# Performance work log

Measured on AMD Instinct MI355X. Metric: run time of the kernel, lower is better.

Reference implementation:

```python
import jax, jax.numpy as jnp
import numpy as np

IN_DIM, HID, E, N = 1024, 2048, 8, 16384

def setup_inputs() -> dict:
    key = jax.random.key(0)
    ks = jax.random.split(key, 12)
    s_in = 1.0 / np.sqrt(IN_DIM)
    s_h = 1.0 / np.sqrt(HID)
    return {
        "x": jax.random.normal(ks[0], (N, IN_DIM), dtype=jnp.float32),
        "enc_W": jax.random.uniform(ks[1], (IN_DIM, HID), jnp.float32, -s_in, s_in),
        "enc_b": jax.random.uniform(ks[2], (HID,), jnp.float32, -s_in, s_in),
        "gate_W": jax.random.uniform(ks[3], (HID, E), jnp.float32, -s_h, s_h),
        "expert_W": jax.random.uniform(ks[4], (E, HID, HID), jnp.float32, -s_h, s_h),
        "expert_b": jax.random.uniform(ks[5], (E, HID), jnp.float32, -s_h, s_h),
        "res_W": jax.random.uniform(ks[6], (HID, HID), jnp.float32, -s_h, s_h),
        "res_b": jax.random.uniform(ks[7], (HID,), jnp.float32, -s_h, s_h),
        "coef_W": jax.random.uniform(ks[8], (HID, 2), jnp.float32, -s_h, s_h),
        "coef_b": jax.random.uniform(ks[9], (2,), jnp.float32, -s_h, s_h),
        "dec_W": jax.random.uniform(ks[10], (HID, IN_DIM), jnp.float32, -s_h, s_h),
        "dec_b": jax.random.uniform(ks[11], (IN_DIM,), jnp.float32, -s_h, s_h),
    }

def reference(x, enc_W, enc_b, gate_W, expert_W, expert_b, res_W, res_b, coef_W, coef_b, dec_W, dec_b):
    # Encode: Linear + ReLU -> h [N, HID]
    h = jax.nn.relu(x @ enc_W + enc_b)
    # Top-1 gating (softmax probs, argmax expert, combine weight = chosen prob)
    probs = jax.nn.softmax(h @ gate_W, axis=-1)          # [N, E]
    idx = jnp.argmax(probs, axis=-1)                     # [N]
    gate = jnp.max(probs, axis=-1, keepdims=True)        # [N, 1]
    # Dense dispatch: run every expert, select via one-hot combine
    y_all = jnp.einsum('nd,edh->neh', h, expert_W) + expert_b  # [N, E, HID]
    onehot = jax.nn.one_hot(idx, y_all.shape[1], dtype=h.dtype)
    moe_out = jnp.einsum('neh,ne->nh', y_all, onehot) * gate   # [N, HID]
    # Residual expert + learned 2-way blending coefficient
    res = h @ res_W + res_b
    coef = jax.nn.softmax(h @ coef_W + coef_b, axis=-1)        # [N, 2]
    out = moe_out * coef[:, 0:1] + res * coef[:, 1:2]
    # Decode
    return out @ dec_W + dec_b
```

## Files before the change

### kernel.cpp

```cpp
#include <hip/hip_runtime.h>


#define N_TOK 16384
#define IN_DIM 1024
#define HID 2048
#define NEXP 8
#define TAU 8.0e-3f

typedef __bf16 bf16_t;
typedef __bf16 bf16x8 __attribute__((ext_vector_type(8)));
typedef __bf16 bf16x4v __attribute__((ext_vector_type(4)));
typedef float f32x4 __attribute__((ext_vector_type(4)));
typedef unsigned short ushort_t;

#define CLAMP1E4(v) fmaxf(fminf((v), 1.0e4f), -1.0e4f)

#define ASYNC16(gp, lp)                                                        \
  __builtin_amdgcn_global_load_lds(                                            \
      (const __attribute__((address_space(1))) void*)(gp),                     \
      (__attribute__((address_space(3))) void*)(lp), 16, 0, 0)

static __device__ inline ushort_t b2u(bf16_t v) {
  union { bf16_t b; ushort_t u; } x; x.b = v; return x.u;
}
// ... 70 lines not shown
    case 5: gWb[i] = (bf16_t)v; break;
    default: cWb[i] = (bf16_t)v; break;
  }
}

__global__ __launch_bounds__(256) void transpose_cvt(
    const void* __restrict__ src0, ushort_t* __restrict__ dst, int R, int C,
    size_t elem_off, const int* __restrict__ flagp, size_t src_zstride,
    size_t dst_zstride) {
  __shared__ ushort_t t[32][33];
  const int f = *flagp;
  const size_t eoff = elem_off + (size_t)blockIdx.z * src_zstride;
  dst += (size_t)blockIdx.z * dst_zstride;
  const int c0 = blockIdx.x * 32, r0 = blockIdx.y * 32;
  const int tx = threadIdx.x, ty = threadIdx.y;
  if (f) {
    const float* s = (const float*)src0 + eoff;
#pragma unroll
    for (int i = 0; i < 4; ++i)
      t[ty + i * 8][tx] =
          b2u((bf16_t)s[(size_t)(r0 + ty + i * 8) * C + c0 + tx]);
  } else {
    const ushort_t* s = (const ushort_t*)src0 + eoff;
#pragma unroll
    for (int i = 0; i < 4; ++i)
      t[ty + i * 8][tx] = s[(size_t)(r0 + ty + i * 8) * C + c0 + tx];
  }
  __syncthreads();
#pragma unroll
  for (int i = 0; i < 4; ++i)
    dst[(size_t)(c0 + ty + i * 8) * R + r0 + tx] = t[tx][ty + i * 8];
}

__global__ __launch_bounds__(256) void enc_gemm(
    const bf16_t* __restrict__ A, const bf16_t* __restrict__ Bt,
    const float* __restrict__ bias, bf16_t* __restrict__ H) {
  __shared__ bf16_t As[128 * 32];
  __shared__ bf16_t Bs[128 * 32];

  const int tid = threadIdx.x, lane = tid & 63, w = tid >> 6;
  const int wr = w >> 1, wc = w & 1, quad = lane >> 4, l16 = lane & 15;
  const int m0 = blockIdx.x * 128, n0 = blockIdx.y * 128;
  const char* Ab = (const char*)A;
  const char* Bb = (const char*)Bt;
  const size_t lda = (size_t)IN_DIM * 2;

  const f32x4 fz = {0.f, 0.f, 0.f, 0.f};
  f32x4 acc[4][4];
#pragma unroll
  for (int i = 0; i < 4; ++i)
#pragma unroll
    for (int j = 0; j < 4; ++j) acc[i][j] = fz;

  size_t aoff[2], boff[2];
  int cb[2];
#pragma unroll
  for (int c = 0; c < 2; ++c) {
    cb[c] = (w * 2 + c) * 1024;
    const int o = cb[c] + lane * 16;
    const int row = o >> 6, kb = o & 63;
    aoff[c] = (size_t)(m0 + row) * lda + kb;
    boff[c] = (size_t)(n0 + row) * lda + kb;
  }

  for (int kt = 0; kt < IN_DIM / 32; ++kt) {
    __syncthreads();
#pragma unroll
    for (int c = 0; c < 2; ++c) {
      ASYNC16(Ab + aoff[c] + (size_t)kt * 64, (char*)As + cb[c]);
      ASYNC16(Bb + boff[c] + (size_t)kt * 64, (char*)Bs + cb[c]);
    }
    __syncthreads();

    bf16x8 af[4], bfr[4];
#pragma unroll
    for (int i = 0; i < 4; ++i)
      af[i] = *(const bf16x8*)&As[(wr * 64 + i * 16 + l16) * 32 + quad * 8];
#pragma unroll
    for (int j = 0; j < 4; ++j)
      bfr[j] = *(const bf16x8*)&Bs[(wc * 64 + j * 16 + l16) * 32 + quad * 8];
#pragma unroll
    for (int i = 0; i < 4; ++i)
#pragma unroll
      for (int j = 0; j < 4; ++j)
        acc[i][j] = __builtin_amdgcn_mfma_f32_16x16x32_bf16(af[i], bfr[j],
                                                            acc[i][j], 0, 0, 0);
  }

  float bj[4];
  int colj[4];
#pragma unroll
  for (int j = 0; j < 4; ++j) {
    colj[j] = n0 + wc * 64 + j * 16 + l16;
    bj[j] = bias[colj[j]];
  }

#pragma unroll
  for (int i = 0; i < 4; ++i) {
#pragma unroll
    for (int r = 0; r < 4; ++r) {
      const int row = m0 + wr * 64 + i * 16 + quad * 4 + r;
#pragma unroll
      for (int j = 0; j < 4; ++j) {
        const float v = fminf(fmaxf(acc[i][j][r] + bj[j], 0.f), 1.0e4f);
        H[(size_t)row * HID + colj[j]] = (bf16_t)v;
      }
    }
  }
}

__global__ __launch_bounds__(256) void gate_from_h(
    const bf16_t* __restrict__ H, const bf16_t* __restrict__ gW,
    const bf16_t* __restrict__ cW, const float* __restrict__ coefBf,
    float* __restrict__ s0g, float* __restrict__ s1g, float* __restrict__ c0g,
    int* __restrict__ eidx, int* __restrict__ ambig, int* __restrict__ acnt,
    int* __restrict__ cnt) {
  const int tid = threadIdx.x, lane = tid & 63, w = tid >> 6;
  const int r0 = blockIdx.x * 16 + w * 4;

// ... 59 lines not shown
#pragma unroll
      for (int e = 0; e < 8; ++e) s += expf(lv[e] - mx);
      const float gate = 1.f / s;
      const float c0 = acc[g][8] + coefBf[0], c1 = acc[g][9] + coefBf[1];
      const float cm = fmaxf(c0, c1);
      const float e0 = expf(c0 - cm), e1 = expf(c1 - cm);
      const float inv = 1.f / (e0 + e1);
      const float p0 = e0 * inv;
      c0g[r] = p0;
      s1g[r] = e1 * inv;
      s0g[r] = gate * p0;
      eidx[r] = idx;
      atomicAdd(&cnt[idx], 1);
      if (mx - s2 < TAU) {
        const int p = atomicAdd(acnt, 1);
        ambig[p] = r;
      }
    }
  }
}

__global__ __launch_bounds__(256) void rescue_rows(
    const void* __restrict__ xraw, const void* __restrict__ encWraw,
    const float* __restrict__ encBf, const void* __restrict__ gateWraw,
    const int* __restrict__ flagp, const int* __restrict__ ambig,
    const int* __restrict__ acnt, const float* __restrict__ c0g,
    float* __restrict__ s0g, int* __restrict__ eidx, int* __restrict__ cnt) {
  const int i = blockIdx.x;
  if (i >= *acnt) return;
  const int r = ambig[i];
  const int f = *flagp;
  const int tid = threadIdx.x;

  double hacc[8] = {0, 0, 0, 0, 0, 0, 0, 0};
  if (f) {
    const float* x = (const float*)xraw + (size_t)r * IN_DIM;
    const float* W = (const float*)encWraw;
    for (int k = 0; k < IN_DIM; ++k) {
      const double xv = (double)x[k];
      const float* Wr = W + (size_t)k * HID;
#pragma unroll
      for (int jj = 0; jj < 8; ++jj)
        hacc[jj] += xv * (double)Wr[tid + jj * 256];
    }
  } else {
    const bf16_t* x = (const bf16_t*)xraw + (size_t)r * IN_DIM;
    const bf16_t* W = (const bf16_t*)encWraw;
    for (int k = 0; k < IN_DIM; ++k) {
      const double xv = (double)(float)x[k];
      const bf16_t* Wr = W + (size_t)k * HID;
#pragma unroll
      for (int jj = 0; jj < 8; ++jj)
        hacc[jj] += xv * (double)(float)Wr[tid + jj * 256];
    }
  }

  double lg[8] = {0, 0, 0, 0, 0, 0, 0, 0};
#pragma unroll
  for (int jj = 0; jj < 8; ++jj) {
    const int j = tid + jj * 256;
    double h = hacc[jj] + (double)encBf[j];
    if (h > 0.0) {
      if (f) {
        const float* g = (const float*)gateWraw + (size_t)j * 8;
#pragma unroll
        for (int e = 0; e < 8; ++e) lg[e] += h * (double)g[e];
      } else {
        const bf16_t* g = (const bf16_t*)gateWraw + (size_t)j * 8;
#pragma unroll
        for (int e = 0; e < 8; ++e) lg[e] += h * (double)(float)g[e];
      }
    }
  }
#pragma unroll
  for (int m = 1; m < 64; m <<= 1)
#pragma unroll
    for (int e = 0; e < 8; ++e) lg[e] += __shfl_xor(lg[e], m);

  __shared__ double red[4][8];
  const int w = tid >> 6, lane = tid & 63;
  if (lane == 0)
#pragma unroll
    for (int e = 0; e < 8; ++e) red[w][e] = lg[e];
  __syncthreads();
  if (tid == 0) {
    double t[8];
// ... 19 lines not shown
}

__global__ __launch_bounds__(256) void place_rows(
    const int* __restrict__ eidx, const int* __restrict__ cnt,
    int* __restrict__ curs, int* __restrict__ permflat) {
  const int r = blockIdx.x * 256 + threadIdx.x;
  const int e = eidx[r];
  int prefix = 0;
  for (int ee = 0; ee < NEXP; ++ee)
    if (ee < e) prefix += cnt[ee];
  const int pos = atomicAdd(&curs[e], 1);
  permflat[prefix + pos] = r;
}

__global__ __launch_bounds__(256) void gather_rows(
    const bf16_t* __restrict__ H, const int* __restrict__ permflat,
    const float* __restrict__ s0g, const float* __restrict__ s1g,
    bf16_t* __restrict__ Hp, int* __restrict__ rowid,
    float* __restrict__ s0p, float* __restrict__ s1p) {
  const int w = threadIdx.x >> 6, lane = threadIdx.x & 63;
  const int p = blockIdx.x * 4 + w;
  const int r = permflat[p];
  if (lane == 0) {
    rowid[p] = r;
    s0p[p] = s0g[r];
    s1p[p] = s1g[r];
  }
  const bf16x8* src = (const bf16x8*)(H + (size_t)r * HID);
  bf16x8* dst = (bf16x8*)(Hp + (size_t)p * HID);
#pragma unroll
  for (int i = 0; i < 4; ++i) dst[lane + i * 64] = src[lane + i * 64];
}

__global__ __launch_bounds__(256) void expert_gemm_t(
    const bf16_t* __restrict__ Hp, const bf16_t* __restrict__ wTall,
    size_t wstride, const float* __restrict__ expBf,
    const int* __restrict__ cnt, const int* __restrict__ rowid,
    const float* __restrict__ s0p, bf16_t* __restrict__ mid) {
  __shared__ bf16_t As[128 * 32];
  __shared__ bf16_t Bs[128 * 32];
  __shared__ int rows_s[128];
  __shared__ float s0_s[128];

  const int x = blockIdx.x;
  int e = -1, base = 0, nrows = 0;
  {
    int acc = 0, pre = 0;
    for (int ee = 0; ee < NEXP; ++ee) {
      const int ce = cnt[ee];
      const int nt = (ce + 127) >> 7;
      if (x < acc + nt) {
        const int t = x - acc;
        e = ee;
        base = pre + t * 128;
        nrows = ce - t * 128;
        if (nrows > 128) nrows = 128;
        break;
      }
      acc += nt;
      pre += ce;
    }
  }
  if (e < 0) return;

  const int tid = threadIdx.x, lane = tid & 63, w = tid >> 6;
  const int wr = w >> 1, wc = w & 1, quad = lane >> 4, l16 = lane & 15;

  if (tid < 128) {
    int grow = -1;
    float a0 = 0.f;
    if (tid < nrows) {
      grow = rowid[base + tid];
      a0 = s0p[base + tid];
    }
    rows_s[tid] = grow;
    s0_s[tid] = a0;
  }
  __syncthreads();

  const int n0 = blockIdx.y * 128;
  const char* Hb = (const char*)Hp;
  const char* Wb = (const char*)(wTall + (size_t)e * wstride);

  size_t aoff[2], boff[2];
  int cb[2];
#pragma unroll
  for (int c = 0; c < 2; ++c) {
    cb[c] = (w * 2 + c) * 1024;
    const int o = cb[c] + lane * 16;
    const int row = o >> 6, kb = o & 63;
    int ar = base + row;
    if (ar > N_TOK - 1) ar = N_TOK - 1;
    aoff[c] = (size_t)ar * (HID * 2) + kb;
    boff[c] = (size_t)(n0 + row) * (HID * 2) + kb;
  }

  const f32x4 fz = {0.f, 0.f, 0.f, 0.f};
  f32x4 acc[4][4];
#pragma unroll
  for (int i = 0; i < 4; ++i)
#pragma unroll
    for (int j = 0; j < 4; ++j) acc[i][j] = fz;

  for (int kt = 0; kt < HID / 32; ++kt) {
    __syncthreads();
#pragma unroll
    for (int c = 0; c < 2; ++c) {
      ASYNC16(Hb + aoff[c] + (size_t)kt * 64, (char*)As + cb[c]);
      ASYNC16(Wb + boff[c] + (size_t)kt * 64, (char*)Bs + cb[c]);
    }
    __syncthreads();

    bf16x8 af[4], bfr[4];
#pragma unroll
    for (int i = 0; i < 4; ++i)
      af[i] = *(const bf16x8*)&As[(wr * 64 + i * 16 + l16) * 32 + quad * 8];
#pragma unroll
    for (int j = 0; j < 4; ++j)
      bfr[j] = *(const bf16x8*)&Bs[(wc * 64 + j * 16 + l16) * 32 + quad * 8];
#pragma unroll
    for (int i = 0; i < 4; ++i)
#pragma unroll
      for (int j = 0; j < 4; ++j)
        acc[i][j] = __builtin_amdgcn_mfma_f32_16x16x32_bf16(af[i], bfr[j],
                                                            acc[i][j], 0, 0, 0);
  }

  const float* eBe = expBf + (size_t)e * HID;
  float beb[4];
  int colj[4];
#pragma unroll
  for (int j = 0; j < 4; ++j) {
    colj[j] = n0 + wc * 64 + j * 16 + l16;
    beb[j] = eBe[colj[j]];
  }
#pragma unroll
  for (int i = 0; i < 4; ++i) {
#pragma unroll
    for (int r = 0; r < 4; ++r) {
      const int lr = wr * 64 + i * 16 + quad * 4 + r;
      const int grow = rows_s[lr];
      if (grow < 0) continue;
      const float s0 = s0_s[lr];
#pragma unroll
      for (int j = 0; j < 4; ++j) {
        const float v = CLAMP1E4(s0 * (acc[i][j][r] + beb[j]));
        mid[(size_t)grow * HID + colj[j]] = (bf16_t)v;
      }
    }
  }
}

__global__ __launch_bounds__(256) void res_gemm_p(
    const bf16_t* __restrict__ Hp, const bf16_t* __restrict__ Bt,
    const float* __restrict__ rB, const int* __restrict__ rowid,
    const float* __restrict__ s1p, bf16_t* __restrict__ mid) {
  __shared__ bf16_t As[128 * 32];
  __shared__ bf16_t Bs[128 * 32];

  const int tid = threadIdx.x, lane = tid & 63, w = tid >> 6;
  const int wr = w >> 1, wc = w & 1, quad = lane >> 4, l16 = lane & 15;
  const int m0 = blockIdx.x * 128, n0 = blockIdx.y * 128;
  const char* Ab = (const char*)Hp;
  const char* Bb = (const char*)Bt;

  size_t aoff[2], boff[2];
  int cb[2];
#pragma unroll
  for (int c = 0; c < 2; ++c) {
    cb[c] = (w * 2 + c) * 1024;
    const int o = cb[c] + lane * 16;
    const int row = o >> 6, kb = o & 63;
    aoff[c] = (size_t)(m0 + row) * (HID * 2) + kb;
    boff[c] = (size_t)(n0 + row) * (HID * 2) + kb;
  }

  const f32x4 fz = {0.f, 0.f, 0.f, 0.f};
  f32x4 acc[4][4];
#pragma unroll
  for (int i = 0; i < 4; ++i)
#pragma unroll
    for (int j = 0; j < 4; ++j) acc[i][j] = fz;

  for (int kt = 0; kt < HID / 32; ++kt) {
    __syncthreads();
#pragma unroll
    for (int c = 0; c < 2; ++c) {
      ASYNC16(Ab + aoff[c] + (size_t)kt * 64, (char*)As + cb[c]);
      ASYNC16(Bb + boff[c] + (size_t)kt * 64, (char*)Bs + cb[c]);
    }
    __syncthreads();

    bf16x8 af[4], bfr[4];
#pragma unroll
    for (int i = 0; i < 4; ++i)
      af[i] = *(const bf16x8*)&As[(wr * 64 + i * 16 + l16) * 32 + quad * 8];
#pragma unroll
    for (int j = 0; j < 4; ++j)
      bfr[j] = *(const bf16x8*)&Bs[(wc * 64 + j * 16 + l16) * 32 + quad * 8];
#pragma unroll
    for (int i = 0; i < 4; ++i)
#pragma unroll
      for (int j = 0; j < 4; ++j)
        acc[i][j] = __builtin_amdgcn_mfma_f32_16x16x32_bf16(af[i], bfr[j],
                                                            acc[i][j], 0, 0, 0);
  }

  float rbb[4];
  int colj[4];
#pragma unroll
  for (int j = 0; j < 4; ++j) {
    colj[j] = n0 + wc * 64 + j * 16 + l16;
    rbb[j] = rB[colj[j]];
  }
#pragma unroll
  for (int i = 0; i < 4; ++i) {
#pragma unroll
    for (int r = 0; r < 4; ++r) {
      const int p = m0 + wr * 64 + i * 16 + quad * 4 + r;
      const int grow = rowid[p];
      const float s1 = s1p[p];
#pragma unroll
      for (int j = 0; j < 4; ++j) {
        const size_t ix = (size_t)grow * HID + colj[j];
        const float v =
            CLAMP1E4(s1 * (acc[i][j][r] + rbb[j]) + (float)mid[ix]);
        mid[ix] = (bf16_t)v;
      }
    }
  }
}

__global__ __launch_bounds__(256) void bucket_rows(
    const int* __restrict__ eidx, int* __restrict__ curs,
    int* __restrict__ perm) {
  const int r = blockIdx.x * 256 + threadIdx.x;
  const int e = eidx[r];
  const int pos = atomicAdd(&curs[e], 1);
  perm[(size_t)e * N_TOK + pos] = r;
}

__global__ __launch_bounds__(256) void expert_gemm(
    const bf16_t* __restrict__ H, const bf16_t* __restrict__ wTe,
    const float* __restrict__ eBe, const int* __restrict__ permE,
    const int* __restrict__ cnt, int e, const float* __restrict__ s0g,
    bf16_t* __restrict__ mid) {
  __shared__ bf16_t As[128 * 32];
  __shared__ bf16_t Bs[128 * 32];
  __shared__ int rows_s[128];
  __shared__ float s0_s[128];

  const int cnte = cnt[e];
  const int lt = blockIdx.x;
  if (lt * 128 >= cnte) return;
  int nrows = cnte - lt * 128;
  if (nrows > 128) nrows = 128;

  const int tid = threadIdx.x, lane = tid & 63, w = tid >> 6;
  const int wr = w >> 1, wc = w & 1, quad = lane >> 4, l16 = lane & 15;

// ... 125 lines not shown
#pragma unroll
    for (int i = 0; i < 4; ++i)
      af[i] = *(const bf16x8*)&As[(wr * 64 + i * 16 + l16) * 32 + quad * 8];
#pragma unroll
    for (int j = 0; j < 4; ++j)
      bfr[j] = *(const bf16x8*)&Bs[(wc * 64 + j * 16 + l16) * 32 + quad * 8];
#pragma unroll
    for (int i = 0; i < 4; ++i)
#pragma unroll
      for (int j = 0; j < 4; ++j)
        acc[i][j] = __builtin_amdgcn_mfma_f32_16x16x32_bf16(af[i], bfr[j],
                                                            acc[i][j], 0, 0, 0);
  }

  float rbb[4];
  int colj[4];
#pragma unroll
  for (int j = 0; j < 4; ++j) {
    colj[j] = n0 + wc * 64 + j * 16 + l16;
    rbb[j] = rB[colj[j]];
  }
#pragma unroll
  for (int i = 0; i < 4; ++i) {
#pragma unroll
    for (int r = 0; r < 4; ++r) {
      const int row = m0 + wr * 64 + i * 16 + quad * 4 + r;
      const float s1 = s1g[row];
#pragma unroll
      for (int j = 0; j < 4; ++j) {
        const size_t ix = (size_t)row * HID + colj[j];
        const float v =
            CLAMP1E4(s1 * (acc[i][j][r] + rbb[j]) + (float)mid[ix]);
        mid[ix] = (bf16_t)v;
      }
    }
  }
}

__global__ __launch_bounds__(256) void dec_gemm(
    const bf16_t* __restrict__ A, const bf16_t* __restrict__ Bt,
    const float* __restrict__ bias, void* __restrict__ C,
    const int* __restrict__ flagp) {
  __shared__ bf16_t As[128 * 32];
  __shared__ bf16_t Bs[128 * 32];

  const int fl = *flagp;
  const int tid = threadIdx.x, lane = tid & 63, w = tid >> 6;
  const int wr = w >> 1, wc = w & 1, quad = lane >> 4, l16 = lane & 15;
  const int m0 = blockIdx.x * 128, n0 = blockIdx.y * 128;
  const char* Ab = (const char*)A;
  const char* Bb = (const char*)Bt;

  size_t aoff[2], boff[2];
  int cb[2];
#pragma unroll
  for (int c = 0; c < 2; ++c) {
    cb[c] = (w * 2 + c) * 1024;
    const int o = cb[c] + lane * 16;
    const int row = o >> 6, kb = o & 63;
    aoff[c] = (size_t)(m0 + row) * (HID * 2) + kb;
    boff[c] = (size_t)(n0 + row) * (HID * 2) + kb;
  }

  const f32x4 fz = {0.f, 0.f, 0.f, 0.f};
  f32x4 acc[4][4];
#pragma unroll
  for (int i = 0; i < 4; ++i)
#pragma unroll
    for (int j = 0; j < 4; ++j) acc[i][j] = fz;

  for (int kt = 0; kt < HID / 32; ++kt) {
    __syncthreads();
#pragma unroll
    for (int c = 0; c < 2; ++c) {
      ASYNC16(Ab + aoff[c] + (size_t)kt * 64, (char*)As + cb[c]);
      ASYNC16(Bb + boff[c] + (size_t)kt * 64, (char*)Bs + cb[c]);
    }
    __syncthreads();

    bf16x8 af[4], bfr[4];
#pragma unroll
    for (int i = 0; i < 4; ++i)
      af[i] = *(const bf16x8*)&As[(wr * 64 + i * 16 + l16) * 32 + quad * 8];
#pragma unroll
    for (int j = 0; j < 4; ++j)
      bfr[j] = *(const bf16x8*)&Bs[(wc * 64 + j * 16 + l16) * 32 + quad * 8];
#pragma unroll
    for (int i = 0; i < 4; ++i)
#pragma unroll
      for (int j = 0; j < 4; ++j)
        acc[i][j] = __builtin_amdgcn_mfma_f32_16x16x32_bf16(af[i], bfr[j],
                                                            acc[i][j], 0, 0, 0);
  }

  float bb[4];
  int colj[4];
#pragma unroll
  for (int j = 0; j < 4; ++j) {
    colj[j] = n0 + wc * 64 + j * 16 + l16;
    bb[j] = bias[colj[j]];
  }
#pragma unroll
  for (int i = 0; i < 4; ++i) {
#pragma unroll
    for (int r = 0; r < 4; ++r) {
      const int row = m0 + wr * 64 + i * 16 + quad * 4 + r;
#pragma unroll
      for (int j = 0; j < 4; ++j) {
        const float v = CLAMP1E4(acc[i][j][r] + bb[j]);
        const size_t ix = (size_t)row * IN_DIM + colj[j];
        if (fl)
          ((float*)C)[ix] = v;
        else
          ((bf16_t*)C)[ix] = (bf16_t)v;
      }
    }
  }
}

extern "C" void kernel_launch(void* const* d_in, const int* in_sizes, int n_in,
                              void* d_out, int out_size, void* d_ws,
                              size_t ws_size, hipStream_t stream) {
  (void)in_sizes; (void)n_in;

  const void* x     = d_in[0];
  const void* encW  = d_in[1];
  const void* encB  = d_in[2];
  const void* gateW = d_in[3];
  const void* expW  = d_in[4];
  const void* expB  = d_in[5];
  const void* resW  = d_in[6];
  const void* resB  = d_in[7];
  const void* coefW = d_in[8];
  const void* coefB = d_in[9];
  const void* decW  = d_in[10];
  const void* decB  = d_in[11];

  char* ws = (char*)d_ws;
  size_t o = 0;
  int*    flag  = (int*)(ws + o);    o += 256;
  int*    cnt   = (int*)(ws + o);    o += 256;
  int*    acnt  = cnt + 8;
  int*    curs  = cnt + 16;
  float*  s0g   = (float*)(ws + o);  o += (size_t)N_TOK * 4;
  float*  s1g   = (float*)(ws + o);  o += (size_t)N_TOK * 4;
  float*  c0g   = (float*)(ws + o);  o += (size_t)N_TOK * 4;
  int*    eidx  = (int*)(ws + o);    o += (size_t)N_TOK * 4;
// ... 36 lines not shown
  cvt_to_bf16_x4<<<dim3(N_TOK * IN_DIM / 4 / 256), 256, 0, stream>>>(
      x, xbf, N_TOK * IN_DIM / 4, flag);
  cvt_small<<<dim3(64, 7), 256, 0, stream>>>(encB, expB, resB, decB, coefB,
                                             gateW, coefW, encBf, expBf, resBf,
                                             decBf, coefBf, gWb, cWb, flag);

  const dim3 tb(32, 8, 1);

  transpose_cvt<<<dim3(HID / 32, IN_DIM / 32, 1), tb, 0, stream>>>(
      encW, (ushort_t*)wT, IN_DIM, HID, 0, flag, 0, 0);
  if (big) {
    transpose_cvt<<<dim3(HID / 32, HID / 32, NEXP), tb, 0, stream>>>(
        expW, (ushort_t*)wTall, HID, HID, 0, flag, S, S);
    transpose_cvt<<<dim3(HID / 32, HID / 32, 1), tb, 0, stream>>>(
        resW, (ushort_t*)(wTall + 8 * S), HID, HID, 0, flag, 0, 0);
    transpose_cvt<<<dim3(IN_DIM / 32, HID / 32, 1), tb, 0, stream>>>(
        decW, (ushort_t*)(wTall + 9 * S), HID, IN_DIM, 0, flag, 0, 0);
  }

  enc_gemm<<<dim3(N_TOK / 128, HID / 128), 256, 0, stream>>>(xbf, wT, encBf,
                                                             hbuf);
  gate_from_h<<<dim3(N_TOK / 16), 256, 0, stream>>>(
      hbuf, gWb, cWb, coefBf, s0g, s1g, c0g, eidx, ambig, acnt, cnt);
  rescue_rows<<<dim3(1024), 256, 0, stream>>>(x, encW, encBf, gateW, flag,
                                              ambig, acnt, c0g, s0g, eidx,
                                              cnt);

  if (big) {
    bf16_t* Hperm = bufB;
    bf16_t* mid   = bufA;
    place_rows<<<dim3(N_TOK / 256), 256, 0, stream>>>(eidx, cnt, curs, permfl);
    gather_rows<<<dim3(N_TOK / 4), 256, 0, stream>>>(hbuf, permfl, s0g, s1g,
                                                     Hperm, rowid, s0p, s1p);
    expert_gemm_t<<<dim3(136, HID / 128), 256, 0, stream>>>(
        Hperm, wTall, S, expBf, cnt, rowid, s0p, mid);
    res_gemm_p<<<dim3(N_TOK / 128, HID / 128), 256, 0, stream>>>(
        Hperm, wTall + 8 * S, resBf, rowid, s1p, mid);
    dec_gemm<<<dim3(N_TOK / 128, IN_DIM / 128), 256, 0, stream>>>(
        mid, wTall + 9 * S, decBf, d_out, flag);
  } else {
    bf16_t* mid = bufB;
    bucket_rows<<<dim3(N_TOK / 256), 256, 0, stream>>>(eidx, curs, perm);
    for (int e = 0; e < NEXP; ++e) {
      transpose_cvt<<<dim3(HID / 32, HID / 32, 1), tb, 0, stream>>>(
          expW, (ushort_t*)wT, HID, HID, (size_t)e * HID * HID, flag, 0, 0);
      expert_gemm<<<dim3(N_TOK / 128, HID / 128), 256, 0, stream>>>(
          hbuf, wT, expBf + (size_t)e * HID, perm + (size_t)e * N_TOK, cnt, e,
          s0g, mid);
    }
    transpose_cvt<<<dim3(HID / 32, HID / 32, 1), tb, 0, stream>>>(
        resW, (ushort_t*)wT, HID, HID, 0, flag, 0, 0);
    res_gemm<<<dim3(N_TOK / 128, HID / 128), 256, 0, stream>>>(hbuf, wT, resBf,
                                                               s1g, mid);
    transpose_cvt<<<dim3(IN_DIM / 32, HID / 32, 1), tb, 0, stream>>>(
        decW, (ushort_t*)wT, HID, IN_DIM, 0, flag, 0, 0);
    dec_gemm<<<dim3(N_TOK / 128, IN_DIM / 128), 256, 0, stream>>>(
        mid, wT, decBf, d_out, flag);
  }
}
```

Baseline: 1.531 ms.

## Fuse expert and residual GEMMs into one kernel sharing the A tile

Merges the routed-expert GEMM and the residual GEMM into a single kernel that loads each permuted-H tile once and accumulates into two sets of MFMA accumulators. The blend is applied in the epilogue, so the read-modify-write of mid in the residual pass and one full re-read of H go away. It also stages x in shared memory and batches weight loads in the fp64 rescue kernel. The cost is doubled accumulator registers, which may lower occupancy, and extra LDS for the second B tile.

```diff
diff --git a/kernel.cpp b/kernel.cpp
--- a/kernel.cpp
+++ b/kernel.cpp
@@ -304,26 +304,50 @@
   const int f = *flagp;
   const int tid = threadIdx.x;
 
+  __shared__ float xs[IN_DIM];
+  if (f) {
+    const float* xp = (const float*)xraw + (size_t)r * IN_DIM;
+    for (int k = tid; k < IN_DIM; k += 256) xs[k] = xp[k];
+  } else {
+    const bf16_t* xp = (const bf16_t*)xraw + (size_t)r * IN_DIM;
+    for (int k = tid; k < IN_DIM; k += 256) xs[k] = (float)xp[k];
+  }
+  __syncthreads();
+
   double hacc[8] = {0, 0, 0, 0, 0, 0, 0, 0};
   if (f) {
-    const float* x = (const float*)xraw + (size_t)r * IN_DIM;
     const float* W = (const float*)encWraw;
-    for (int k = 0; k < IN_DIM; ++k) {
-      const double xv = (double)x[k];
-      const float* Wr = W + (size_t)k * HID;
-#pragma unroll
-      for (int jj = 0; jj < 8; ++jj)
-        hacc[jj] += xv * (double)Wr[tid + jj * 256];
+    for (int k0 = 0; k0 < IN_DIM; k0 += 8) {
+      float wv[8][8];
+#pragma unroll
+      for (int kk = 0; kk < 8; ++kk) {
+        const float* Wr = W + (size_t)(k0 + kk) * HID + tid;
+#pragma unroll
+        for (int jj = 0; jj < 8; ++jj) wv[kk][jj] = Wr[jj * 256];
+      }
+#pragma unroll
+      for (int kk = 0; kk < 8; ++kk) {
+        const double xv = (double)xs[k0 + kk];
+#pragma unroll
+        for (int jj = 0; jj < 8; ++jj) hacc[jj] += xv * (double)wv[kk][jj];
+      }
     }
   } else {
-    const bf16_t* x = (const bf16_t*)xraw + (size_t)r * IN_DIM;
     const bf16_t* W = (const bf16_t*)encWraw;
-    for (int k = 0; k < IN_DIM; ++k) {
-      const double xv = (double)(float)x[k];
-      const bf16_t* Wr = W + (size_t)k * HID;
-#pragma unroll
-      for (int jj = 0; jj < 8; ++jj)
-        hacc[jj] += xv * (double)(float)Wr[tid + jj * 256];
+    for (int k0 = 0; k0 < IN_DIM; k0 += 8) {
+      float wv[8][8];
+#pragma unroll
+      for (int kk = 0; kk < 8; ++kk) {
+        const bf16_t* Wr = W + (size_t)(k0 + kk) * HID + tid;
+#pragma unroll
+        for (int jj = 0; jj < 8; ++jj) wv[kk][jj] = (float)Wr[jj * 256];
+      }
+#pragma unroll
+      for (int kk = 0; kk < 8; ++kk) {
+        const double xv = (double)xs[k0 + kk];
+#pragma unroll
+        for (int jj = 0; jj < 8; ++jj) hacc[jj] += xv * (double)wv[kk][jj];
+      }
     }
   }
 
@@ -409,15 +433,18 @@
   for (int i = 0; i < 4; ++i) dst[lane + i * 64] = src[lane + i * 64];
 }
 
-__global__ __launch_bounds__(256) void expert_gemm_t(
+__global__ __launch_bounds__(256) void expert_res_gemm(
     const bf16_t* __restrict__ Hp, const bf16_t* __restrict__ wTall,
     size_t wstride, const float* __restrict__ expBf,
-    const int* __restrict__ cnt, const int* __restrict__ rowid,
-    const float* __restrict__ s0p, bf16_t* __restrict__ mid) {
+    const float* __restrict__ rB, const int* __restrict__ cnt,
+    const int* __restrict__ rowid, const float* __restrict__ s0p,
+    const float* __restrict__ s1p, bf16_t* __restrict__ mid) {
   __shared__ bf16_t As[128 * 32];
-  __shared__ bf16_t Bs[128 * 32];
+  __shared__ bf16_t Bse[128 * 32];
+  __shared__ bf16_t Bsr[128 * 32];
   __shared__ int rows_s[128];
   __shared__ float s0_s[128];
+  __shared__ float s1_s[128];
 
   const int x = blockIdx.x;
   int e = -1, base = 0, nrows = 0;
@@ -445,19 +472,22 @@
 
   if (tid < 128) {
     int grow = -1;
-    float a0 = 0.f;
+    float a0 = 0.f, a1 = 0.f;
     if (tid < nrows) {
       grow = rowid[base + tid];
       a0 = s0p[base + tid];
+      a1 = s1p[base + tid];
     }
     rows_s[tid] = grow;
     s0_s[tid] = a0;
+    s1_s[tid] = a1;
   }
   __syncthreads();
 
   const int n0 = blockIdx.y * 128;
   const char* Hb = (const char*)Hp;
-  const char* Wb = (const char*)(wTall + (size_t)e * wstride);
+  const char* We = (const char*)(wTall + (size_t)e * wstride);
+  const char* Wr = (const char*)(wTall + (size_t)8 * wstride);
 
   size_t aoff[2], boff[2];
   int cb[2];
@@ -473,43 +503,55 @@
   }
 
   const f32x4 fz = {0.f, 0.f, 0.f, 0.f};
-  f32x4 acc[4][4];
+  f32x4 acce[4][4], accr[4][4];
 #pragma unroll
   for (int i = 0; i < 4; ++i)
 #pragma unroll
-    for (int j = 0; j < 4; ++j) acc[i][j] = fz;
+    for (int j = 0; j < 4; ++j) {
+      acce[i][j] = fz;
+      accr[i][j] = fz;
+    }
 
   for (int kt = 0; kt < HID / 32; ++kt) {
     __syncthreads();
 #pragma unroll
     for (int c = 0; c < 2; ++c) {
       ASYNC16(Hb + aoff[c] + (size_t)kt * 64, (char*)As + cb[c]);
-      ASYNC16(Wb + boff[c] + (size_t)kt * 64, (char*)Bs + cb[c]);
+      ASYNC16(We + boff[c] + (size_t)kt * 64, (char*)Bse + cb[c]);
+      ASYNC16(Wr + boff[c] + (size_t)kt * 64, (char*)Bsr + cb[c]);
     }
     __syncthreads();
 
-    bf16x8 af[4], bfr[4];
+    bf16x8 af[4], bfe[4], bfr[4];
 #pragma unroll
     for (int i = 0; i < 4; ++i)
       af[i] = *(const bf16x8*)&As[(wr * 64 + i * 16 + l16) * 32 + quad * 8];
 #pragma unroll
-    for (int j = 0; j < 4; ++j)
-      bfr[j] = *(const bf16x8*)&Bs[(wc * 64 + j * 16 + l16) * 32 + quad * 8];
-#pragma unroll
-    for (int i = 0; i < 4; ++i)
-#pragma unroll
-      for (int j = 0; j < 4; ++j)
-        acc[i][j] = __builtin_amdgcn_mfma_f32_16x16x32_bf16(af[i], bfr[j],
-                                                            acc[i][j], 0, 0, 0);
+    for (int j = 0; j < 4; ++j) {
+      bfe[j] = *(const bf16x8*)&Bse[(wc * 64 + j * 16 + l16) * 32 + quad * 8];
+      bfr[j] = *(const bf16x8*)&Bsr[(wc * 64 + j * 16 + l16) * 32 + quad * 8];
+    }
+#pragma unroll
+    for (int i = 0; i < 4; ++i)
+#pragma unroll
+      for (int j = 0; j < 4; ++j) {
+        acce[i][j] = __builtin_amdgcn_mfma_f32_16x16x32_bf16(af[i], bfe[j],
+                                                             acce[i][j], 0, 0,
+                                                             0);
+        accr[i][j] = __builtin_amdgcn_mfma_f32_16x16x32_bf16(af[i], bfr[j],
+                                                             accr[i][j], 0, 0,
+                                                             0);
+      }
   }
 
   const float* eBe = expBf + (size_t)e * HID;
-  float beb[4];
+  float beb[4], rbb[4];
   int colj[4];
 #pragma unroll
   for (int j = 0; j < 4; ++j) {
     colj[j] = n0 + wc * 64 + j * 16 + l16;
     beb[j] = eBe[colj[j]];
+    rbb[j] = rB[colj[j]];
   }
 #pragma unroll
   for (int i = 0; i < 4; ++i) {
@@ -519,90 +561,12 @@
       const int grow = rows_s[lr];
       if (grow < 0) continue;
       const float s0 = s0_s[lr];
+      const float s1 = s1_s[lr];
 #pragma unroll
       for (int j = 0; j < 4; ++j) {
-        const float v = CLAMP1E4(s0 * (acc[i][j][r] + beb[j]));
+        const float v = CLAMP1E4(s0 * (acce[i][j][r] + beb[j]) +
+                                 s1 * (accr[i][j][r] + rbb[j]));
         mid[(size_t)grow * HID + colj[j]] = (bf16_t)v;
-      }
-    }
-  }
-}
-
-__global__ __launch_bounds__(256) void res_gemm_p(
-    const bf16_t* __restrict__ Hp, const bf16_t* __restrict__ Bt,
-    const float* __restrict__ rB, const int* __restrict__ rowid,
-    const float* __restrict__ s1p, bf16_t* __restrict__ mid) {
-  __shared__ bf16_t As[128 * 32];
-  __shared__ bf16_t Bs[128 * 32];
-
-  const int tid = threadIdx.x, lane = tid & 63, w = tid >> 6;
-  const int wr = w >> 1, wc = w & 1, quad = lane >> 4, l16 = lane & 15;
-  const int m0 = blockIdx.x * 128, n0 = blockIdx.y * 128;
-  const char* Ab = (const char*)Hp;
-  const char* Bb = (const char*)Bt;
-
-  size_t aoff[2], boff[2];
-  int cb[2];
-#pragma unroll
-  for (int c = 0; c < 2; ++c) {
-    cb[c] = (w * 2 + c) * 1024;
-    const int o = cb[c] + lane * 16;
-    const int row = o >> 6, kb = o & 63;
-    aoff[c] = (size_t)(m0 + row) * (HID * 2) + kb;
-    boff[c] = (size_t)(n0 + row) * (HID * 2) + kb;
-  }
-
-  const f32x4 fz = {0.f, 0.f, 0.f, 0.f};
-  f32x4 acc[4][4];
-#pragma unroll
-  for (int i = 0; i < 4; ++i)
-#pragma unroll
-    for (int j = 0; j < 4; ++j) acc[i][j] = fz;
-
-  for (int kt = 0; kt < HID / 32; ++kt) {
-    __syncthreads();
-#pragma unroll
-    for (int c = 0; c < 2; ++c) {
-      ASYNC16(Ab + aoff[c] + (size_t)kt * 64, (char*)As + cb[c]);
-      ASYNC16(Bb + boff[c] + (size_t)kt * 64, (char*)Bs + cb[c]);
-    }
-    __syncthreads();
-
-    bf16x8 af[4], bfr[4];
-#pragma unroll
-    for (int i = 0; i < 4; ++i)
-      af[i] = *(const bf16x8*)&As[(wr * 64 + i * 16 + l16) * 32 + quad * 8];
-#pragma unroll
-    for (int j = 0; j < 4; ++j)
-      bfr[j] = *(const bf16x8*)&Bs[(wc * 64 + j * 16 + l16) * 32 + quad * 8];
-#pragma unroll
-    for (int i = 0; i < 4; ++i)
-#pragma unroll
-      for (int j = 0; j < 4; ++j)
-        acc[i][j] = __builtin_amdgcn_mfma_f32_16x16x32_bf16(af[i], bfr[j],
-                                                            acc[i][j], 0, 0, 0);
-  }
-
-  float rbb[4];
-  int colj[4];
-#pragma unroll
-  for (int j = 0; j < 4; ++j) {
-    colj[j] = n0 + wc * 64 + j * 16 + l16;
-    rbb[j] = rB[colj[j]];
-  }
-#pragma unroll
-  for (int i = 0; i < 4; ++i) {
-#pragma unroll
-    for (int r = 0; r < 4; ++r) {
-      const int p = m0 + wr * 64 + i * 16 + quad * 4 + r;
-      const int grow = rowid[p];
-      const float s1 = s1p[p];
-#pragma unroll
-      for (int j = 0; j < 4; ++j) {
-        const size_t ix = (size_t)grow * HID + colj[j];
-        const float v =
-            CLAMP1E4(s1 * (acc[i][j][r] + rbb[j]) + (float)mid[ix]);
-        mid[ix] = (bf16_t)v;
       }
     }
   }
@@ -977,10 +941,8 @@
     place_rows<<<dim3(N_TOK / 256), 256, 0, stream>>>(eidx, cnt, curs, permfl);
     gather_rows<<<dim3(N_TOK / 4), 256, 0, stream>>>(hbuf, permfl, s0g, s1g,
                                                      Hperm, rowid, s0p, s1p);
-    expert_gemm_t<<<dim3(136, HID / 128), 256, 0, stream>>>(
-        Hperm, wTall, S, expBf, cnt, rowid, s0p, mid);
-    res_gemm_p<<<dim3(N_TOK / 128, HID / 128), 256, 0, stream>>>(
-        Hperm, wTall + 8 * S, resBf, rowid, s1p, mid);
+    expert_res_gemm<<<dim3(136, HID / 128), 256, 0, stream>>>(
+        Hperm, wTall, S, expBf, resBf, cnt, rowid, s0p, s1p, mid);
     dec_gemm<<<dim3(N_TOK / 128, IN_DIM / 128), 256, 0, stream>>>(
         mid, wTall + 9 * S, decBf, d_out, flag);
   } else {
```

Result: slower. 1.735 ms (+13.4%).

## Double GEMM K-tile to 64 with XOR-swizzled LDS and batch rescue-row loads

Applied to the files above, without the earlier changes.

All four MFMA GEMMs (encoder, expert, residual, decoder) now stage a 64-wide K slice per iteration instead of 32. This halves the number of barrier pairs per tile, and an XOR swizzle on the LDS layout avoids the bank conflicts that the wider row stride would otherwise cause. The fp64 rescue kernel now caches the input row in shared memory and loads weights in 8x8 register batches for more memory-level parallelism. The cost is double the LDS per block, which may lower occupancy, and more registers.

```diff
diff --git a/kernel.cpp b/kernel.cpp
--- a/kernel.cpp
+++ b/kernel.cpp
@@ -126,11 +126,12 @@
     dst[(size_t)(c0 + ty + i * 8) * R + r0 + tx] = t[tx][ty + i * 8];
 }
 
+
 __global__ __launch_bounds__(256) void enc_gemm(
     const bf16_t* __restrict__ A, const bf16_t* __restrict__ Bt,
     const float* __restrict__ bias, bf16_t* __restrict__ H) {
-  __shared__ bf16_t As[128 * 32];
-  __shared__ bf16_t Bs[128 * 32];
+  __shared__ bf16_t As[128 * 64];
+  __shared__ bf16_t Bs[128 * 64];
 
   const int tid = threadIdx.x, lane = tid & 63, w = tid >> 6;
   const int wr = w >> 1, wc = w & 1, quad = lane >> 4, l16 = lane & 15;
@@ -146,39 +147,45 @@
 #pragma unroll
     for (int j = 0; j < 4; ++j) acc[i][j] = fz;
 
-  size_t aoff[2], boff[2];
-  int cb[2];
-#pragma unroll
-  for (int c = 0; c < 2; ++c) {
-    cb[c] = (w * 2 + c) * 1024;
+  size_t aoff[4], boff[4];
+  int cb[4];
+#pragma unroll
+  for (int c = 0; c < 4; ++c) {
+    cb[c] = (w * 4 + c) * 1024;
     const int o = cb[c] + lane * 16;
-    const int row = o >> 6, kb = o & 63;
+    const int row = o >> 7;
+    const int kb = (o & 127) ^ ((row & 7) << 4);
     aoff[c] = (size_t)(m0 + row) * lda + kb;
     boff[c] = (size_t)(n0 + row) * lda + kb;
   }
-
-  for (int kt = 0; kt < IN_DIM / 32; ++kt) {
-    __syncthreads();
-#pragma unroll
-    for (int c = 0; c < 2; ++c) {
-      ASYNC16(Ab + aoff[c] + (size_t)kt * 64, (char*)As + cb[c]);
-      ASYNC16(Bb + boff[c] + (size_t)kt * 64, (char*)Bs + cb[c]);
-    }
-    __syncthreads();
-
-    bf16x8 af[4], bfr[4];
-#pragma unroll
-    for (int i = 0; i < 4; ++i)
-      af[i] = *(const bf16x8*)&As[(wr * 64 + i * 16 + l16) * 32 + quad * 8];
-#pragma unroll
-    for (int j = 0; j < 4; ++j)
-      bfr[j] = *(const bf16x8*)&Bs[(wc * 64 + j * 16 + l16) * 32 + quad * 8];
-#pragma unroll
-    for (int i = 0; i < 4; ++i)
+  const int sw = (l16 & 7) << 3;
+
+  for (int kt = 0; kt < IN_DIM / 64; ++kt) {
+    __syncthreads();
+#pragma unroll
+    for (int c = 0; c < 4; ++c) {
+      ASYNC16(Ab + aoff[c] + (size_t)kt * 128, (char*)As + cb[c]);
+      ASYNC16(Bb + boff[c] + (size_t)kt * 128, (char*)Bs + cb[c]);
+    }
+    __syncthreads();
+
+#pragma unroll
+    for (int ks = 0; ks < 2; ++ks) {
+      const int co = (ks * 32 + quad * 8) ^ sw;
+      bf16x8 af[4], bfr[4];
+#pragma unroll
+      for (int i = 0; i < 4; ++i)
+        af[i] = *(const bf16x8*)&As[(wr * 64 + i * 16 + l16) * 64 + co];
 #pragma unroll
       for (int j = 0; j < 4; ++j)
-        acc[i][j] = __builtin_amdgcn_mfma_f32_16x16x32_bf16(af[i], bfr[j],
-                                                            acc[i][j], 0, 0, 0);
+        bfr[j] = *(const bf16x8*)&Bs[(wc * 64 + j * 16 + l16) * 64 + co];
+#pragma unroll
+      for (int i = 0; i < 4; ++i)
+#pragma unroll
+        for (int j = 0; j < 4; ++j)
+          acc[i][j] = __builtin_amdgcn_mfma_f32_16x16x32_bf16(
+              af[i], bfr[j], acc[i][j], 0, 0, 0);
+    }
   }
 
   float bj[4];
@@ -304,26 +311,50 @@
   const int f = *flagp;
   const int tid = threadIdx.x;
 
+  __shared__ float xs[IN_DIM];
+  if (f) {
+    const float* xp = (const float*)xraw + (size_t)r * IN_DIM;
+    for (int k = tid; k < IN_DIM; k += 256) xs[k] = xp[k];
+  } else {
+    const bf16_t* xp = (const bf16_t*)xraw + (size_t)r * IN_DIM;
+    for (int k = tid; k < IN_DIM; k += 256) xs[k] = (float)xp[k];
+  }
+  __syncthreads();
+
   double hacc[8] = {0, 0, 0, 0, 0, 0, 0, 0};
   if (f) {
-    const float* x = (const float*)xraw + (size_t)r * IN_DIM;
     const float* W = (const float*)encWraw;
-    for (int k = 0; k < IN_DIM; ++k) {
-      const double xv = (double)x[k];
-      const float* Wr = W + (size_t)k * HID;
-#pragma unroll
-      for (int jj = 0; jj < 8; ++jj)
-        hacc[jj] += xv * (double)Wr[tid + jj * 256];
+    for (int k0 = 0; k0 < IN_DIM; k0 += 8) {
+      float wv[8][8];
+#pragma unroll
+      for (int kk = 0; kk < 8; ++kk) {
+        const float* Wr = W + (size_t)(k0 + kk) * HID + tid;
+#pragma unroll
+        for (int jj = 0; jj < 8; ++jj) wv[kk][jj] = Wr[jj * 256];
+      }
+#pragma unroll
+      for (int kk = 0; kk < 8; ++kk) {
+        const double xv = (double)xs[k0 + kk];
+#pragma unroll
+        for (int jj = 0; jj < 8; ++jj) hacc[jj] += xv * (double)wv[kk][jj];
+      }
     }
   } else {
-    const bf16_t* x = (const bf16_t*)xraw + (size_t)r * IN_DIM;
     const bf16_t* W = (const bf16_t*)encWraw;
-    for (int k = 0; k < IN_DIM; ++k) {
-      const double xv = (double)(float)x[k];
-      const bf16_t* Wr = W + (size_t)k * HID;
-#pragma unroll
-      for (int jj = 0; jj < 8; ++jj)
-        hacc[jj] += xv * (double)(float)Wr[tid + jj * 256];
+    for (int k0 = 0; k0 < IN_DIM; k0 += 8) {
+      float wv[8][8];
+#pragma unroll
+      for (int kk = 0; kk < 8; ++kk) {
+        const bf16_t* Wr = W + (size_t)(k0 + kk) * HID + tid;
+#pragma unroll
+        for (int jj = 0; jj < 8; ++jj) wv[kk][jj] = (float)Wr[jj * 256];
+      }
+#pragma unroll
+      for (int kk = 0; kk < 8; ++kk) {
+        const double xv = (double)xs[k0 + kk];
+#pragma unroll
+        for (int jj = 0; jj < 8; ++jj) hacc[jj] += xv * (double)wv[kk][jj];
+      }
     }
   }
 
@@ -414,8 +445,8 @@
     size_t wstride, const float* __restrict__ expBf,
     const int* __restrict__ cnt, const int* __restrict__ rowid,
     const float* __restrict__ s0p, bf16_t* __restrict__ mid) {
-  __shared__ bf16_t As[128 * 32];
-  __shared__ bf16_t Bs[128 * 32];
+  __shared__ bf16_t As[128 * 64];
+  __shared__ bf16_t Bs[128 * 64];
   __shared__ int rows_s[128];
   __shared__ float s0_s[128];
 
@@ -459,18 +490,20 @@
   const char* Hb = (const char*)Hp;
   const char* Wb = (const char*)(wTall + (size_t)e * wstride);
 
-  size_t aoff[2], boff[2];
-  int cb[2];
-#pragma unroll
-  for (int c = 0; c < 2; ++c) {
-    cb[c] = (w * 2 + c) * 1024;
+  size_t aoff[4], boff[4];
+  int cb[4];
+#pragma unroll
+  for (int c = 0; c < 4; ++c) {
+    cb[c] = (w * 4 + c) * 1024;
     const int o = cb[c] + lane * 16;
-    const int row = o >> 6, kb = o & 63;
+    const int row = o >> 7;
+    const int kb = (o & 127) ^ ((row & 7) << 4);
     int ar = base + row;
     if (ar > N_TOK - 1) ar = N_TOK - 1;
     aoff[c] = (size_t)ar * (HID * 2) + kb;
     boff[c] = (size_t)(n0 + row) * (HID * 2) + kb;
   }
+  const int sw = (l16 & 7) << 3;
 
   const f32x4 fz = {0.f, 0.f, 0.f, 0.f};
   f32x4 acc[4][4];
@@ -479,28 +512,32 @@
 #pragma unroll
     for (int j = 0; j < 4; ++j) acc[i][j] = fz;
 
-  for (int kt = 0; kt < HID / 32; ++kt) {
-    __syncthreads();
-#pragma unroll
-    for (int c = 0; c < 2; ++c) {
-      ASYNC16(Hb + aoff[c] + (size_t)kt * 64, (char*)As + cb[c]);
-      ASYNC16(Wb + boff[c] + (size_t)kt * 64, (char*)Bs + cb[c]);
-    }
-    __syncthreads();
-
-    bf16x8 af[4], bfr[4];
-#pragma unroll
-    for (int i = 0; i < 4; ++i)
-      af[i] = *(const bf16x8*)&As[(wr * 64 + i * 16 + l16) * 32 + quad * 8];
-#pragma unroll
-    for (int j = 0; j < 4; ++j)
-      bfr[j] = *(const bf16x8*)&Bs[(wc * 64 + j * 16 + l16) * 32 + quad * 8];
-#pragma unroll
-    for (int i = 0; i < 4; ++i)
+  for (int kt = 0; kt < HID / 64; ++kt) {
+    __syncthreads();
+#pragma unroll
+    for (int c = 0; c < 4; ++c) {
+      ASYNC16(Hb + aoff[c] + (size_t)kt * 128, (char*)As + cb[c]);
+      ASYNC16(Wb + boff[c] + (size_t)kt * 128, (char*)Bs + cb[c]);
+    }
+    __syncthreads();
+
+#pragma unroll
+    for (int ks = 0; ks < 2; ++ks) {
+      const int co = (ks * 32 + quad * 8) ^ sw;
+      bf16x8 af[4], bfr[4];
+#pragma unroll
+      for (int i = 0; i < 4; ++i)
+        af[i] = *(const bf16x8*)&As[(wr * 64 + i * 16 + l16) * 64 + co];
 #pragma unroll
       for (int j = 0; j < 4; ++j)
-        acc[i][j] = __builtin_amdgcn_mfma_f32_16x16x32_bf16(af[i], bfr[j],
-                                                            acc[i][j], 0, 0, 0);
+        bfr[j] = *(const bf16x8*)&Bs[(wc * 64 + j * 16 + l16) * 64 + co];
+#pragma unroll
+      for (int i = 0; i < 4; ++i)
+#pragma unroll
+        for (int j = 0; j < 4; ++j)
+          acc[i][j] = __builtin_amdgcn_mfma_f32_16x16x32_bf16(
+              af[i], bfr[j], acc[i][j], 0, 0, 0);
+    }
   }
 
   const float* eBe = expBf + (size_t)e * HID;
@@ -532,8 +569,8 @@
     const bf16_t* __restrict__ Hp, const bf16_t* __restrict__ Bt,
     const float* __restrict__ rB, const int* __restrict__ rowid,
     const float* __restrict__ s1p, bf16_t* __restrict__ mid) {
-  __shared__ bf16_t As[128 * 32];
-  __shared__ bf16_t Bs[128 * 32];
+  __shared__ bf16_t As[128 * 64];
+  __shared__ bf16_t Bs[128 * 64];
 
   const int tid = threadIdx.x, lane = tid & 63, w = tid >> 6;
   const int wr = w >> 1, wc = w & 1, quad = lane >> 4, l16 = lane & 15;
@@ -541,16 +578,18 @@
   const char* Ab = (const char*)Hp;
   const char* Bb = (const char*)Bt;
 
-  size_t aoff[2], boff[2];
-  int cb[2];
-#pragma unroll
-  for (int c = 0; c < 2; ++c) {
-    cb[c] = (w * 2 + c) * 1024;
+  size_t aoff[4], boff[4];
+  int cb[4];
+#pragma unroll
+  for (int c = 0; c < 4; ++c) {
+    cb[c] = (w * 4 + c) * 1024;
     const int o = cb[c] + lane * 16;
-    const int row = o >> 6, kb = o & 63;
+    const int row = o >> 7;
+    const int kb = (o & 127) ^ ((row & 7) << 4);
     aoff[c] = (size_t)(m0 + row) * (HID * 2) + kb;
     boff[c] = (size_t)(n0 + row) * (HID * 2) + kb;
   }
+  const int sw = (l16 & 7) << 3;
 
   const f32x4 fz = {0.f, 0.f, 0.f, 0.f};
   f32x4 acc[4][4];
@@ -559,28 +598,32 @@
 #pragma unroll
     for (int j = 0; j < 4; ++j) acc[i][j] = fz;
 
-  for (int kt = 0; kt < HID / 32; ++kt) {
-    __syncthreads();
-#pragma unroll
-    for (int c = 0; c < 2; ++c) {
-      ASYNC16(Ab + aoff[c] + (size_t)kt * 64, (char*)As + cb[c]);
-      ASYNC16(Bb + boff[c] + (size_t)kt * 64, (char*)Bs + cb[c]);
-    }
-    __syncthreads();
-
-    bf16x8 af[4], bfr[4];
-#pragma unroll
-    for (int i = 0; i < 4; ++i)
-      af[i] = *(const bf16x8*)&As[(wr * 64 + i * 16 + l16) * 32 + quad * 8];
-#pragma unroll
-    for (int j = 0; j < 4; ++j)
-      bfr[j] = *(const bf16x8*)&Bs[(wc * 64 + j * 16 + l16) * 32 + quad * 8];
-#pragma unroll
-    for (int i = 0; i < 4; ++i)
+  for (int kt = 0; kt < HID / 64; ++kt) {
+    __syncthreads();
+#pragma unroll
+    for (int c = 0; c < 4; ++c) {
+      ASYNC16(Ab + aoff[c] + (size_t)kt * 128, (char*)As + cb[c]);
+      ASYNC16(Bb + boff[c] + (size_t)kt * 128, (char*)Bs + cb[c]);
+    }
+    __syncthreads();
+
+#pragma unroll
+    for (int ks = 0; ks < 2; ++ks) {
+      const int co = (ks * 32 + quad * 8) ^ sw;
+      bf16x8 af[4], bfr[4];
+#pragma unroll
+      for (int i = 0; i < 4; ++i)
+        af[i] = *(const bf16x8*)&As[(wr * 64 + i * 16 + l16) * 64 + co];
 #pragma unroll
       for (int j = 0; j < 4; ++j)
-        acc[i][j] = __builtin_amdgcn_mfma_f32_16x16x32_bf16(af[i], bfr[j],
-                                                            acc[i][j], 0, 0, 0);
+        bfr[j] = *(const bf16x8*)&Bs[(wc * 64 + j * 16 + l16) * 64 + co];
+#pragma unroll
+      for (int i = 0; i < 4; ++i)
+#pragma unroll
+        for (int j = 0; j < 4; ++j)
+          acc[i][j] = __builtin_amdgcn_mfma_f32_16x16x32_bf16(
+              af[i], bfr[j], acc[i][j], 0, 0, 0);
+    }
   }
 
   float rbb[4];
@@ -603,6 +646,93 @@
         const float v =
             CLAMP1E4(s1 * (acc[i][j][r] + rbb[j]) + (float)mid[ix]);
         mid[ix] = (bf16_t)v;
+      }
+    }
+  }
+}
+
+__global__ __launch_bounds__(256) void dec_gemm(
+    const bf16_t* __restrict__ A, const bf16_t* __restrict__ Bt,
+    const float* __restrict__ bias, void* __restrict__ C,
+    const int* __restrict__ flagp) {
+  __shared__ bf16_t As[128 * 64];
+  __shared__ bf16_t Bs[128 * 64];
+
+  const int fl = *flagp;
+  const int tid = threadIdx.x, lane = tid & 63, w = tid >> 6;
+  const int wr = w >> 1, wc = w & 1, quad = lane >> 4, l16 = lane & 15;
+  const int m0 = blockIdx.x * 128, n0 = blockIdx.y * 128;
+  const char* Ab = (const char*)A;
+  const char* Bb = (const char*)Bt;
+
+  size_t aoff[4], boff[4];
+  int cb[4];
+#pragma unroll
+  for (int c = 0; c < 4; ++c) {
+    cb[c] = (w * 4 + c) * 1024;
+    const int o = cb[c] + lane * 16;
+    const int row = o >> 7;
+    const int kb = (o & 127) ^ ((row & 7) << 4);
+    aoff[c] = (size_t)(m0 + row) * (HID * 2) + kb;
+    boff[c] = (size_t)(n0 + row) * (HID * 2) + kb;
+  }
+  const int sw = (l16 & 7) << 3;
+
+  const f32x4 fz = {0.f, 0.f, 0.f, 0.f};
+  f32x4 acc[4][4];
+#pragma unroll
+  for (int i = 0; i < 4; ++i)
+#pragma unroll
+    for (int j = 0; j < 4; ++j) acc[i][j] = fz;
+
+  for (int kt = 0; kt < HID / 64; ++kt) {
+    __syncthreads();
+#pragma unroll
+    for (int c = 0; c < 4; ++c) {
+      ASYNC16(Ab + aoff[c] + (size_t)kt * 128, (char*)As + cb[c]);
+      ASYNC16(Bb + boff[c] + (size_t)kt * 128, (char*)Bs + cb[c]);
+    }
+    __syncthreads();
+
+#pragma unroll
+    for (int ks = 0; ks < 2; ++ks) {
+      const int co = (ks * 32 + quad * 8) ^ sw;
+      bf16x8 af[4], bfr[4];
+#pragma unroll
+      for (int i = 0; i < 4; ++i)
+        af[i] = *(const bf16x8*)&As[(wr * 64 + i * 16 + l16) * 64 + co];
+#pragma unroll
+      for (int j = 0; j < 4; ++j)
+        bfr[j] = *(const bf16x8*)&Bs[(wc * 64 + j * 16 + l16) * 64 + co];
+#pragma unroll
+      for (int i = 0; i < 4; ++i)
+#pragma unroll
+        for (int j = 0; j < 4; ++j)
+          acc[i][j] = __builtin_amdgcn_mfma_f32_16x16x32_bf16(
+              af[i], bfr[j], acc[i][j], 0, 0, 0);
+    }
+  }
+
+  float bb[4];
+  int colj[4];
+#pragma unroll
+  for (int j = 0; j < 4; ++j) {
+    colj[j] = n0 + wc * 64 + j * 16 + l16;
+    bb[j] = bias[colj[j]];
+  }
+#pragma unroll
+  for (int i = 0; i < 4; ++i) {
+#pragma unroll
+    for (int r = 0; r < 4; ++r) {
+      const int row = m0 + wr * 64 + i * 16 + quad * 4 + r;
+#pragma unroll
+      for (int j = 0; j < 4; ++j) {
+        const float v = CLAMP1E4(acc[i][j][r] + bb[j]);
+        const size_t ix = (size_t)row * IN_DIM + colj[j];
+        if (fl)
+          ((float*)C)[ix] = v;
+        else
+          ((bf16_t*)C)[ix] = (bf16_t)v;
       }
     }
   }
@@ -794,87 +924,6 @@
         const float v =
             CLAMP1E4(s1 * (acc[i][j][r] + rbb[j]) + (float)mid[ix]);
         mid[ix] = (bf16_t)v;
-      }
-    }
-  }
-}
-
-__global__ __launch_bounds__(256) void dec_gemm(
-    const bf16_t* __restrict__ A, const bf16_t* __restrict__ Bt,
-    const float* __restrict__ bias, void* __restrict__ C,
-    const int* __restrict__ flagp) {
-  __shared__ bf16_t As[128 * 32];
-  __shared__ bf16_t Bs[128 * 32];
-
-  const int fl = *flagp;
-  const int tid = threadIdx.x, lane = tid & 63, w = tid >> 6;
-  const int wr = w >> 1, wc = w & 1, quad = lane >> 4, l16 = lane & 15;
-  const int m0 = blockIdx.x * 128, n0 = blockIdx.y * 128;
-  const char* Ab = (const char*)A;
-  const char* Bb = (const char*)Bt;
-
-  size_t aoff[2], boff[2];
-  int cb[2];
-#pragma unroll
-  for (int c = 0; c < 2; ++c) {
-    cb[c] = (w * 2 + c) * 1024;
-    const int o = cb[c] + lane * 16;
-    const int row = o >> 6, kb = o & 63;
-    aoff[c] = (size_t)(m0 + row) * (HID * 2) + kb;
-    boff[c] = (size_t)(n0 + row) * (HID * 2) + kb;
-  }
-
-  const f32x4 fz = {0.f, 0.f, 0.f, 0.f};
-  f32x4 acc[4][4];
-#pragma unroll
-  for (int i = 0; i < 4; ++i)
-#pragma unroll
-    for (int j = 0; j < 4; ++j) acc[i][j] = fz;
-
-  for (int kt = 0; kt < HID / 32; ++kt) {
-    __syncthreads();
-#pragma unroll
-    for (int c = 0; c < 2; ++c) {
-      ASYNC16(Ab + aoff[c] + (size_t)kt * 64, (char*)As + cb[c]);
-      ASYNC16(Bb + boff[c] + (size_t)kt * 64, (char*)Bs + cb[c]);
-    }
-    __syncthreads();
-
-    bf16x8 af[4], bfr[4];
-#pragma unroll
-    for (int i = 0; i < 4; ++i)
-      af[i] = *(const bf16x8*)&As[(wr * 64 + i * 16 + l16) * 32 + quad * 8];
-#pragma unroll
-    for (int j = 0; j < 4; ++j)
-      bfr[j] = *(const bf16x8*)&Bs[(wc * 64 + j * 16 + l16) * 32 + quad * 8];
-#pragma unroll
-    for (int i = 0; i < 4; ++i)
-#pragma unroll
-      for (int j = 0; j < 4; ++j)
-        acc[i][j] = __builtin_amdgcn_mfma_f32_16x16x32_bf16(af[i], bfr[j],
-                                                            acc[i][j], 0, 0, 0);
-  }
-
-  float bb[4];
-  int colj[4];
-#pragma unroll
-  for (int j = 0; j < 4; ++j) {
-    colj[j] = n0 + wc * 64 + j * 16 + l16;
-    bb[j] = bias[colj[j]];
-  }
-#pragma unroll
-  for (int i = 0; i < 4; ++i) {
-#pragma unroll
-    for (int r = 0; r < 4; ++r) {
-      const int row = m0 + wr * 64 + i * 16 + quad * 4 + r;
-#pragma unroll
-      for (int j = 0; j < 4; ++j) {
-        const float v = CLAMP1E4(acc[i][j][r] + bb[j]);
-        const size_t ix = (size_t)row * IN_DIM + colj[j];
-        if (fl)
-          ((float*)C)[ix] = v;
-        else
-          ((bf16_t*)C)[ix] = (bf16_t)v;
       }
     }
   }
```

After: 1.534 ms. No clear change (+0.2%).
